# Kernel tuning notes

Hardware: AMD Instinct MI355X
Metric: run time of the kernel (lower is better)

The kernel has to match this reference:

```python
import jax, jax.numpy as jnp
import numpy as np

B = 65536
FEAT = 64
NUM_CONT = 2
NUM_DISC = FEAT - NUM_CONT  # 62
D = 16                      # embedding_size
H1, H2 = 256, 128           # hidden_dims
DNN_IN = FEAT * D           # 1024


def setup_inputs() -> dict:
    key = jax.random.key(0)
    ks = jax.random.split(key, 12)
    # x: first NUM_DISC cols are binary category ids (stored as float), last NUM_CONT are 'continuous'
    x = jax.random.randint(ks[0], (B, FEAT), 0, 2).astype(jnp.float32)
    s = 0.05
    return {
        "x": x,
        # 62 embedding tables of shape (2, D), stacked: [NUM_DISC, 2, D]
        "emb_tables": jax.random.normal(ks[1], (NUM_DISC, 2, D), jnp.float32) * s,
        "Wc": jax.random.normal(ks[2], (NUM_CONT * D, NUM_CONT), jnp.float32) * s,  # cont_linear
        "bc": jnp.zeros((NUM_CONT * D,), jnp.float32),
        "Wf": jax.random.normal(ks[3], (1, FEAT), jnp.float32) * s,                 # fm_linear
        "bf": jnp.zeros((1,), jnp.float32),
        "W1": jax.random.normal(ks[4], (H1, DNN_IN), jnp.float32) * s,
        "b1": jnp.zeros((H1,), jnp.float32),
        "W2": jax.random.normal(ks[5], (H2, H1), jnp.float32) * s,
        "b2": jnp.zeros((H2,), jnp.float32),
    }


def reference(x, emb_tables, Wc, bc, Wf, bf, W1, b1, W2, b2):
    # --- embeddings ---
    disc_idx = x[:, :NUM_DISC].astype(jnp.int32)                     # [B, 62]
    # per-feature table gather: emb_tables[f, idx[b,f]] -> [B, 62, D]
    disc_embeds = emb_tables[jnp.arange(NUM_DISC)[None, :], disc_idx]
    cont = x[:, NUM_DISC:]                                           # [B, 2]
    cont_embeds = (cont @ Wc.T + bc).reshape(-1, NUM_CONT, D)        # [B, 2, D]
    all_embeds = jnp.concatenate([disc_embeds, cont_embeds], axis=1) # [B, 64, D]

    # --- FM first order ---
    fm_first = x @ Wf.T + bf                                         # [B, 1]

    # --- FM second order: sum_{i<j} <e_i, e_j> = 0.5 * ((sum_i e_i)^2 - sum_i e_i^2) summed over D
    sum_e = jnp.sum(all_embeds, axis=1)                              # [B, D]
    sum_sq = jnp.sum(all_embeds * all_embeds, axis=(1, 2))           # [B]
    fm_second = 0.5 * (jnp.sum(sum_e * sum_e, axis=1) - sum_sq)      # [B]
    fm_second = fm_second[:, None]                                   # [B, 1]

    # --- DNN ---
    h = all_embeds.reshape(x.shape[0], -1)                           # [B, 1024]
    h = jax.nn.relu(h @ W1.T + b1)                                   # [B, 256]
    h = jax.nn.relu(h @ W2.T + b2)                                   # [B, 128]

    return jnp.concatenate([fm_first + fm_second, h], axis=1)        # [B, 129]
```

## Files before the change

### kernel.cpp

```cpp
#include <hip/hip_runtime.h>
#include <hip/hip_bf16.h>


#define NROWS   65536
#define NFEAT   64
#define NDISC   62
#define DIM     16
#define K1      1024
#define H1N     256
#define H2N     128
#define OUTC    129

using f32x4  = __attribute__((ext_vector_type(4))) float;
using bf16x8 = __attribute__((ext_vector_type(8))) short;

__device__ __forceinline__ unsigned short f2bf(float f) {
    unsigned u = __builtin_bit_cast(unsigned, f);
    u = (u + 0x7FFFu + ((u >> 16) & 1u)) >> 16;
    return (unsigned short)u;
}

__device__ __forceinline__ void async16(const void* g, void* l) {
    __builtin_amdgcn_global_load_lds(
        (const __attribute__((address_space(1))) void*)g,
        (__attribute__((address_space(3))) void*)l, 16, 0, 0);
}

__global__ __launch_bounds__(256) void convert_w(const float* __restrict__ W1,
                                                 const float* __restrict__ W2,
                                                 unsigned short* __restrict__ W1b,
                                                 unsigned short* __restrict__ W2b) {
    int i = blockIdx.x * 256 + threadIdx.x;
    if (i < H1N * K1) W1b[i] = f2bf(W1[i]);
    if (i < H2N * H1N) W2b[i] = f2bf(W2[i]);
}

__global__ __launch_bounds__(256) void fm_kernel(const float* __restrict__ x,
                                                 const float* __restrict__ tbl,
                                                 const float* __restrict__ Wc,
                                                 const float* __restrict__ bc,
                                                 const float* __restrict__ Wf,
                                                 const float* __restrict__ bfp,
                                                 float* __restrict__ out) {
    __shared__ float tblL[NDISC * 2 * DIM];
    __shared__ float WcL[64];
    __shared__ float bcL[32];
    __shared__ float WfL[64];
    const int t = threadIdx.x, l = t & 63, w = t >> 6;
    const int d = l & 15;
    for (int i = t; i < NDISC * 2 * DIM; i += 256) tblL[i] = tbl[i];
    if (t < 64) WcL[t] = Wc[t];
    else if (t < 96) bcL[t - 64] = bc[t - 64];
    else if (t < 160) WfL[t - 96] = Wf[t - 96];
    __syncthreads();
    const float bf0 = bfp[0];

    const int waveId = blockIdx.x * 4 + w;
    #pragma unroll
    for (int it = 0; it < 2; ++it) {
        const int grp = waveId + it * 8192;
        const int row = grp * 4 + (l >> 4);
        const float4 v = *(const float4*)(x + (size_t)row * NFEAT + d * 4);

        unsigned long long m =
            ((unsigned long long)((int)v.x & 1)) |
            ((unsigned long long)((int)v.y & 1) << 1) |
            ((unsigned long long)((int)v.z & 1) << 2) |
            ((unsigned long long)((int)v.w & 1) << 3);
        m <<= (d * 4);
        m |= __shfl_xor(m, 1); m |= __shfl_xor(m, 2);
        m |= __shfl_xor(m, 4); m |= __shfl_xor(m, 8);
        const float c0 = __shfl(v.z, l | 15);
        const float c1 = __shfl(v.w, l | 15);

        float fp = v.x * WfL[4 * d] + v.y * WfL[4 * d + 1] +
                   v.z * WfL[4 * d + 2] + v.w * WfL[4 * d + 3];

        float se = 0.f, ssq = 0.f;
        #pragma unroll
        for (int f = 0; f < NDISC; ++f) {
            const int bit = (int)((m >> f) & 1ULL);
            const float e = tblL[(f * 2 + bit) * DIM + d];
            se += e; ssq += e * e;
        }
        {
            const float e62 = bcL[d]      + c0 * WcL[2 * d]            + c1 * WcL[2 * d + 1];
            const float e63 = bcL[16 + d] + c0 * WcL[2 * (16 + d)]     + c1 * WcL[2 * (16 + d) + 1];
            se += e62 + e63; ssq += e62 * e62 + e63 * e63;
        }

        float u = se * se - ssq;
        u  += __shfl_xor(u, 1);  u  += __shfl_xor(u, 2);
        u  += __shfl_xor(u, 4);  u  += __shfl_xor(u, 8);
        fp += __shfl_xor(fp, 1); fp += __shfl_xor(fp, 2);
        fp += __shfl_xor(fp, 4); fp += __shfl_xor(fp, 8);
        if (d == 0) out[(size_t)row * OUTC] = fp + bf0 + 0.5f * u;
    }
}

__global__ __launch_bounds__(512, 4) void gemm1_fused(
        const float* __restrict__ x,
        const float* __restrict__ tbl,
        const float* __restrict__ Wc,
        const float* __restrict__ bc,
        const unsigned short* __restrict__ W1b,
        const float* __restrict__ b1,
        unsigned short* __restrict__ H1b) {
    __shared__ unsigned short ldsA[128 * 64];
    __shared__ unsigned short ldsB[256 * 64];
    __shared__ unsigned char  xb[128 * 64];
    __shared__ float contf[128 * 2];
    __shared__ unsigned short tblLb[NDISC * 2 * DIM];
    __shared__ float WcL[64];
    __shared__ float bcL[32];

    const int t  = threadIdx.x;
    const int l  = t & 63;
    const int w  = t >> 6;
    const int wr = w >> 2;
    const int wc = w & 3;
    const int m0 = blockIdx.x * 128;

    for (int i = t; i < NDISC * 2 * DIM; i += 512) tblLb[i] = f2bf(tbl[i]);
    if (t < 64) WcL[t] = Wc[t];
    if (t >= 64 && t < 96) bcL[t - 64] = bc[t - 64];

    {
        const int row = t >> 2, cbase = (t & 3) * 16;
        const float4* xp = (const float4*)(x + (size_t)(m0 + row) * NFEAT + cbase);
        #pragma unroll
        for (int q = 0; q < 4; ++q) {
            float4 v = xp[q];
            unsigned pk = ((unsigned)(int)v.x) | ((unsigned)(int)v.y << 8) |
                          ((unsigned)(int)v.z << 16) | ((unsigned)(int)v.w << 24);
            *(unsigned*)&xb[row * 64 + cbase + q * 4] = pk;
            if (cbase + q * 4 == 60) {
                contf[row * 2]     = v.z;
                contf[row * 2 + 1] = v.w;
            }
        }
    }
    __syncthreads();

    f32x4 acc[4][4] = {};

    for (int ks = 0; ks < 16; ++ks) {
        const int k0 = ks * 64;
        const int f0 = ks * 4;

        #pragma unroll
        for (int p = 0; p < 2; ++p) {
            const int chunk = p * 512 + t;
            const int row = chunk >> 3;
            const int cc  = chunk & 7;
            const int fl  = cc >> 1;
            const int d0  = (cc & 1) * 8;
            const int f   = f0 + fl;
            bf16x8 pk;
            if (f < NDISC) {
                const int bit = xb[row * 64 + f] & 1;
                pk = *(const bf16x8*)&tblLb[(f * 2 + bit) * DIM + d0];
            } else {
                const float c0v = contf[row * 2], c1v = contf[row * 2 + 1];
                const int j0 = (f - NDISC) * 16 + d0;
                #pragma unroll
                for (int dd = 0; dd < 8; ++dd) {
                    const int j = j0 + dd;
                    pk[dd] = (short)f2bf(bcL[j] + c0v * WcL[2 * j] + c1v * WcL[2 * j + 1]);
                }
            }
            *(bf16x8*)&ldsA[row * 64 + (cc ^ (row & 7)) * 8] = pk;
        }

        {
            unsigned short* dstbase = &ldsB[0] + w * 512;
            #pragma unroll
            for (int p = 0; p < 4; ++p) {
                const int chunk = p * 512 + t;
                const int row = chunk >> 3;
                const int cc  = chunk & 7;
                const int ccs = cc ^ (row & 7);
                async16(W1b + (size_t)row * K1 + k0 + ccs * 8, dstbase + p * 4096);
            }
        }
        __syncthreads();

        #pragma unroll
        for (int sub = 0; sub < 2; ++sub) {
            const int s = sub * 4 + (l >> 4);
            bf16x8 af[4], bfr[4];
            #pragma unroll
            for (int i = 0; i < 4; ++i) {
                const int ra = wr * 64 + i * 16 + (l & 15);
                af[i] = *(const bf16x8*)&ldsA[ra * 64 + (s ^ (ra & 7)) * 8];
            }
            #pragma unroll
            for (int j = 0; j < 4; ++j) {
                const int rb = wc * 64 + j * 16 + (l & 15);
                bfr[j] = *(const bf16x8*)&ldsB[rb * 64 + (s ^ (rb & 7)) * 8];
            }
            #pragma unroll
            for (int i = 0; i < 4; ++i)
                #pragma unroll
                for (int j = 0; j < 4; ++j)
                    acc[i][j] = __builtin_amdgcn_mfma_f32_16x16x32_bf16(af[i], bfr[j], acc[i][j], 0, 0, 0);
        }
        __syncthreads();
    }

    #pragma unroll
    for (int i = 0; i < 4; ++i) {
        const int rbase = m0 + wr * 64 + i * 16 + (l >> 4) * 4;
        #pragma unroll
        for (int j = 0; j < 4; ++j) {
            const int col = wc * 64 + j * 16 + (l & 15);
            const float bias = b1[col];
            #pragma unroll
            for (int r = 0; r < 4; ++r) {
                float v = acc[i][j][r] + bias;
                v = v > 0.f ? v : 0.f;
                H1b[(size_t)(rbase + r) * H1N + col] = f2bf(v);
            }
        }
    }
}

__global__ __launch_bounds__(256, 2) void gemm2_k(
        const unsigned short* __restrict__ H1b,
        const unsigned short* __restrict__ W2b,
        const float* __restrict__ b2,
        float* __restrict__ out) {
    __shared__ unsigned short ldsA[128 * 128];
    __shared__ unsigned short ldsB[128 * 128];
    const int t = threadIdx.x, l = t & 63, w = t >> 6;
    const int wr = w >> 1, wc = w & 1;
    const int m0 = blockIdx.x * 128;

    f32x4 acc[4][4] = {};

    for (int ks = 0; ks < 2; ++ks) {
        const int k0 = ks * 128;
        {
            unsigned short* da = &ldsA[0] + w * 512;
            unsigned short* db = &ldsB[0] + w * 512;
            #pragma unroll
            for (int p = 0; p < 8; ++p) {
                const int chunk = p * 256 + t;
                const int row = chunk >> 4;
                const int cc  = chunk & 15;
                const int ccs = cc ^ (row & 7);
                async16(H1b + (size_t)(m0 + row) * H1N + k0 + ccs * 8, da + p * 2048);
            }
            #pragma unroll
            for (int p = 0; p < 8; ++p) {
                const int chunk = p * 256 + t;
                const int row = chunk >> 4;
                const int cc  = chunk & 15;
                const int ccs = cc ^ (row & 7);
                async16(W2b + (size_t)row * H1N + k0 + ccs * 8, db + p * 2048);
            }
        }
        __syncthreads();
        #pragma unroll
        for (int sub = 0; sub < 4; ++sub) {
            const int s = sub * 4 + (l >> 4);
            bf16x8 af[4], bfr[4];
            #pragma unroll
            for (int i = 0; i < 4; ++i) {
                const int ra = wr * 64 + i * 16 + (l & 15);
                af[i] = *(const bf16x8*)&ldsA[ra * 128 + (s ^ (ra & 7)) * 8];
            }
            #pragma unroll
            for (int j = 0; j < 4; ++j) {
                const int rb = wc * 64 + j * 16 + (l & 15);
                bfr[j] = *(const bf16x8*)&ldsB[rb * 128 + (s ^ (rb & 7)) * 8];
            }
            #pragma unroll
            for (int i = 0; i < 4; ++i)
                #pragma unroll
                for (int j = 0; j < 4; ++j)
                    acc[i][j] = __builtin_amdgcn_mfma_f32_16x16x32_bf16(af[i], bfr[j], acc[i][j], 0, 0, 0);
        }
        __syncthreads();
    }

    #pragma unroll
    for (int i = 0; i < 4; ++i) {
        const int rbase = m0 + wr * 64 + i * 16 + (l >> 4) * 4;
        #pragma unroll
        for (int j = 0; j < 4; ++j) {
            const int n = wc * 64 + j * 16 + (l & 15);
            const float bias = b2[n];
            #pragma unroll
            for (int r = 0; r < 4; ++r) {
                float v = acc[i][j][r] + bias;
                v = v > 0.f ? v : 0.f;
                out[(size_t)(rbase + r) * OUTC + 1 + n] = v;
            }
        }
    }
}

extern "C" void kernel_launch(void* const* d_in, const int* in_sizes, int n_in,
                              void* d_out, int out_size, void* d_ws, size_t ws_size,
                              hipStream_t stream) {
    const float* x   = (const float*)d_in[0];
    const float* tbl = (const float*)d_in[1];
    const float* Wc  = (const float*)d_in[2];
    const float* bc  = (const float*)d_in[3];
    const float* Wf  = (const float*)d_in[4];
    const float* bfp = (const float*)d_in[5];
    const float* W1  = (const float*)d_in[6];
    const float* b1  = (const float*)d_in[7];
    const float* W2  = (const float*)d_in[8];
    const float* b2  = (const float*)d_in[9];
    float* out = (float*)d_out;

    char* ws = (char*)d_ws;
    unsigned short* W1b = (unsigned short*)ws;
    unsigned short* W2b = (unsigned short*)(ws + 524288);
    unsigned short* H1b = (unsigned short*)(ws + 589824);

    convert_w<<<dim3(H1N * K1 / 256), dim3(256), 0, stream>>>(W1, W2, W1b, W2b);
    fm_kernel<<<dim3(2048), dim3(256), 0, stream>>>(x, tbl, Wc, bc, Wf, bfp, out);
    gemm1_fused<<<dim3(NROWS / 128), dim3(512), 0, stream>>>(x, tbl, Wc, bc, W1b, b1, H1b);
    gemm2_k<<<dim3(NROWS / 128), dim3(256), 0, stream>>>(H1b, W2b, b2, out);
}
```

Before: 146.3 us.

## Fuse second GEMM into first GEMM kernel via LDS-resident H1 tile

Merges the two MLP layers into one kernel. The relu'd H1 tile (128x256 bf16) is written to a swizzled region of shared memory that reuses the A/B staging buffers. The second GEMM then reads W2 fragments straight from global memory. This removes the H1 round trip through global memory and one kernel launch. In exchange, shared memory use rises to a single 64KB block, which may limit occupancy, and W2 is read from global/L2 by every block without LDS staging.

```diff
diff --git a/kernel.cpp b/kernel.cpp
--- a/kernel.cpp
+++ b/kernel.cpp
@@ -84,8 +84,8 @@
             se += e; ssq += e * e;
         }
         {
-            const float e62 = bcL[d]      + c0 * WcL[2 * d]            + c1 * WcL[2 * d + 1];
-            const float e63 = bcL[16 + d] + c0 * WcL[2 * (16 + d)]     + c1 * WcL[2 * (16 + d) + 1];
+            const float e62 = bcL[d]      + c0 * WcL[2 * d]        + c1 * WcL[2 * d + 1];
+            const float e63 = bcL[16 + d] + c0 * WcL[2 * (16 + d)] + c1 * WcL[2 * (16 + d) + 1];
             se += e62 + e63; ssq += e62 * e62 + e63 * e63;
         }
 
@@ -98,21 +98,25 @@
     }
 }
 
-__global__ __launch_bounds__(512, 4) void gemm1_fused(
+__global__ __launch_bounds__(512, 4) void gemm_fused(
         const float* __restrict__ x,
         const float* __restrict__ tbl,
         const float* __restrict__ Wc,
         const float* __restrict__ bc,
         const unsigned short* __restrict__ W1b,
         const float* __restrict__ b1,
-        unsigned short* __restrict__ H1b) {
-    __shared__ unsigned short ldsA[128 * 64];
-    __shared__ unsigned short ldsB[256 * 64];
-    __shared__ unsigned char  xb[128 * 64];
-    __shared__ float contf[128 * 2];
-    __shared__ unsigned short tblLb[NDISC * 2 * DIM];
-    __shared__ float WcL[64];
-    __shared__ float bcL[32];
+        const unsigned short* __restrict__ W2b,
+        const float* __restrict__ b2,
+        float* __restrict__ out) {
+    __shared__ __align__(16) char smem[65536];
+    unsigned short* ldsA  = (unsigned short*)(smem);
+    unsigned short* ldsB  = (unsigned short*)(smem + 16384);
+    unsigned char*  xb    = (unsigned char*)(smem + 49152);
+    float*          contf = (float*)(smem + 57344);
+    unsigned short* tblLb = (unsigned short*)(smem + 58368);
+    float*          WcL   = (float*)(smem + 62336);
+    float*          bcL   = (float*)(smem + 62592);
+    unsigned short* H1t   = (unsigned short*)(smem);
 
     const int t  = threadIdx.x;
     const int l  = t & 63;
@@ -173,7 +177,7 @@
         }
 
         {
-            unsigned short* dstbase = &ldsB[0] + w * 512;
+            unsigned short* dstbase = ldsB + w * 512;
             #pragma unroll
             for (int p = 0; p < 4; ++p) {
                 const int chunk = p * 512 + t;
@@ -210,90 +214,53 @@
 
     #pragma unroll
     for (int i = 0; i < 4; ++i) {
-        const int rbase = m0 + wr * 64 + i * 16 + (l >> 4) * 4;
+        const int rloc0 = wr * 64 + i * 16 + (l >> 4) * 4;
         #pragma unroll
         for (int j = 0; j < 4; ++j) {
-            const int col = wc * 64 + j * 16 + (l & 15);
+            const int col  = wc * 64 + j * 16 + (l & 15);
+            const int slot = col >> 3, cin = col & 7;
             const float bias = b1[col];
             #pragma unroll
             for (int r = 0; r < 4; ++r) {
+                const int row = rloc0 + r;
                 float v = acc[i][j][r] + bias;
                 v = v > 0.f ? v : 0.f;
-                H1b[(size_t)(rbase + r) * H1N + col] = f2bf(v);
-            }
-        }
-    }
-}
-
-__global__ __launch_bounds__(256, 2) void gemm2_k(
-        const unsigned short* __restrict__ H1b,
-        const unsigned short* __restrict__ W2b,
-        const float* __restrict__ b2,
-        float* __restrict__ out) {
-    __shared__ unsigned short ldsA[128 * 128];
-    __shared__ unsigned short ldsB[128 * 128];
-    const int t = threadIdx.x, l = t & 63, w = t >> 6;
-    const int wr = w >> 1, wc = w & 1;
-    const int m0 = blockIdx.x * 128;
-
-    f32x4 acc[4][4] = {};
-
-    for (int ks = 0; ks < 2; ++ks) {
-        const int k0 = ks * 128;
-        {
-            unsigned short* da = &ldsA[0] + w * 512;
-            unsigned short* db = &ldsB[0] + w * 512;
-            #pragma unroll
-            for (int p = 0; p < 8; ++p) {
-                const int chunk = p * 256 + t;
-                const int row = chunk >> 4;
-                const int cc  = chunk & 15;
-                const int ccs = cc ^ (row & 7);
-                async16(H1b + (size_t)(m0 + row) * H1N + k0 + ccs * 8, da + p * 2048);
-            }
-            #pragma unroll
-            for (int p = 0; p < 8; ++p) {
-                const int chunk = p * 256 + t;
-                const int row = chunk >> 4;
-                const int cc  = chunk & 15;
-                const int ccs = cc ^ (row & 7);
-                async16(W2b + (size_t)row * H1N + k0 + ccs * 8, db + p * 2048);
-            }
-        }
-        __syncthreads();
-        #pragma unroll
-        for (int sub = 0; sub < 4; ++sub) {
-            const int s = sub * 4 + (l >> 4);
-            bf16x8 af[4], bfr[4];
-            #pragma unroll
-            for (int i = 0; i < 4; ++i) {
-                const int ra = wr * 64 + i * 16 + (l & 15);
-                af[i] = *(const bf16x8*)&ldsA[ra * 128 + (s ^ (ra & 7)) * 8];
-            }
-            #pragma unroll
-            for (int j = 0; j < 4; ++j) {
-                const int rb = wc * 64 + j * 16 + (l & 15);
-                bfr[j] = *(const bf16x8*)&ldsB[rb * 128 + (s ^ (rb & 7)) * 8];
-            }
-            #pragma unroll
-            for (int i = 0; i < 4; ++i)
-                #pragma unroll
-                for (int j = 0; j < 4; ++j)
-                    acc[i][j] = __builtin_amdgcn_mfma_f32_16x16x32_bf16(af[i], bfr[j], acc[i][j], 0, 0, 0);
-        }
-        __syncthreads();
-    }
-
-    #pragma unroll
-    for (int i = 0; i < 4; ++i) {
-        const int rbase = m0 + wr * 64 + i * 16 + (l >> 4) * 4;
-        #pragma unroll
-        for (int j = 0; j < 4; ++j) {
-            const int n = wc * 64 + j * 16 + (l & 15);
+                H1t[row * 256 + (slot ^ (row & 7)) * 8 + cin] = f2bf(v);
+            }
+        }
+    }
+    __syncthreads();
+
+    f32x4 acc2[4][2] = {};
+    #pragma unroll
+    for (int kk = 0; kk < 8; ++kk) {
+        bf16x8 bfr2[2];
+        #pragma unroll
+        for (int j2 = 0; j2 < 2; ++j2) {
+            const int nrow = wc * 32 + j2 * 16 + (l & 15);
+            bfr2[j2] = *(const bf16x8*)(W2b + (size_t)nrow * H1N + kk * 32 + (l >> 4) * 8);
+        }
+        const int slot = kk * 4 + (l >> 4);
+        #pragma unroll
+        for (int i2 = 0; i2 < 4; ++i2) {
+            const int ra = wr * 64 + i2 * 16 + (l & 15);
+            const bf16x8 af2 = *(const bf16x8*)&H1t[ra * 256 + (slot ^ (ra & 7)) * 8];
+            #pragma unroll
+            for (int j2 = 0; j2 < 2; ++j2)
+                acc2[i2][j2] = __builtin_amdgcn_mfma_f32_16x16x32_bf16(af2, bfr2[j2], acc2[i2][j2], 0, 0, 0);
+        }
+    }
+
+    #pragma unroll
+    for (int i2 = 0; i2 < 4; ++i2) {
+        const int rbase = m0 + wr * 64 + i2 * 16 + (l >> 4) * 4;
+        #pragma unroll
+        for (int j2 = 0; j2 < 2; ++j2) {
+            const int n = wc * 32 + j2 * 16 + (l & 15);
             const float bias = b2[n];
             #pragma unroll
             for (int r = 0; r < 4; ++r) {
-                float v = acc[i][j][r] + bias;
+                float v = acc2[i2][j2][r] + bias;
                 v = v > 0.f ? v : 0.f;
                 out[(size_t)(rbase + r) * OUTC + 1 + n] = v;
             }
@@ -319,10 +286,9 @@
     char* ws = (char*)d_ws;
     unsigned short* W1b = (unsigned short*)ws;
     unsigned short* W2b = (unsigned short*)(ws + 524288);
-    unsigned short* H1b = (unsigned short*)(ws + 589824);
 
     convert_w<<<dim3(H1N * K1 / 256), dim3(256), 0, stream>>>(W1, W2, W1b, W2b);
     fm_kernel<<<dim3(2048), dim3(256), 0, stream>>>(x, tbl, Wc, bc, Wf, bfp, out);
-    gemm1_fused<<<dim3(NROWS / 128), dim3(512), 0, stream>>>(x, tbl, Wc, bc, W1b, b1, H1b);
-    gemm2_k<<<dim3(NROWS / 128), dim3(256), 0, stream>>>(H1b, W2b, b2, out);
-}
+    gemm_fused<<<dim3(NROWS / 128), dim3(512), 0, stream>>>(x, tbl, Wc, bc, W1b, b1,
+                                                            W2b, b2, out);
+}
```

Measured after the change: 140.3 us. 4.1% less time.
